# Optimization experiments

Measured on AMD Instinct MI355X. Metric: run time of the kernel, lower is better.

Reference implementation:

```python
import jax, jax.numpy as jnp
import numpy as np

N_NODES = 100000
N_EDGES = 1600000
N_GRAPHS = 256
NODE_DIM = 64
EDGE_DIM = 64
HIDDEN = 128
VOCAB = 128
N_CONV = 3
R_MIN, R_MAX = 1.0, 6.0
LN_EPS = 1e-5


def layer_norm(x, g, b):
    mu = jnp.mean(x, axis=-1, keepdims=True)
    var = jnp.mean(jnp.square(x - mu), axis=-1, keepdims=True)
    return (x - mu) * jax.lax.rsqrt(var + LN_EPS) * g + b


def setup_inputs() -> dict:
    key = jax.random.key(0)
    ks = jax.random.split(key, 16)
    inp = {}
    inp["numbers"] = jax.random.randint(ks[0], (N_NODES,), 0, VOCAB)
    inp["edge_index"] = jax.random.randint(ks[1], (2, N_EDGES), 0, N_NODES)
    inp["edge_length"] = jax.random.uniform(ks[2], (N_EDGES,), minval=R_MIN, maxval=R_MAX, dtype=jnp.float32)
    inp["batch"] = jnp.sort(jax.random.randint(ks[3], (N_NODES,), 0, N_GRAPHS))
    s = 0.1
    inp["embed_table"] = jax.random.normal(ks[4], (VOCAB, NODE_DIM), jnp.float32)
    inp["Wf"] = jax.random.normal(ks[5], (N_CONV, 2 * NODE_DIM + EDGE_DIM, NODE_DIM), jnp.float32) * s
    inp["bf"] = jnp.zeros((N_CONV, NODE_DIM), jnp.float32)
    inp["Ws"] = jax.random.normal(ks[6], (N_CONV, 2 * NODE_DIM + EDGE_DIM, NODE_DIM), jnp.float32) * s
    inp["bs"] = jnp.zeros((N_CONV, NODE_DIM), jnp.float32)
    inp["ln_g"] = jnp.ones((N_CONV, NODE_DIM), jnp.float32)
    inp["ln_b"] = jnp.zeros((N_CONV, NODE_DIM), jnp.float32)
    inp["olp_W1"] = jax.random.normal(ks[7], (NODE_DIM, HIDDEN), jnp.float32) * s
    inp["olp_b1"] = jnp.zeros((HIDDEN,), jnp.float32)
    inp["olp_g1"] = jnp.ones((HIDDEN,), jnp.float32)
    inp["olp_bt1"] = jnp.zeros((HIDDEN,), jnp.float32)
    inp["olp_W2"] = jax.random.normal(ks[8], (HIDDEN, HIDDEN), jnp.float32) * s
    inp["olp_b2"] = jnp.zeros((HIDDEN,), jnp.float32)
    inp["olp_g2"] = jnp.ones((HIDDEN,), jnp.float32)
    inp["olp_bt2"] = jnp.zeros((HIDDEN,), jnp.float32)
    inp["W_out"] = jax.random.normal(ks[9], (HIDDEN, 1), jnp.float32) * s
    inp["b_out"] = jnp.zeros((1,), jnp.float32)
    return inp


def reference(numbers, edge_index, edge_length, batch, embed_table,
              Wf, bf, Ws, bs, ln_g, ln_b,
              olp_W1, olp_b1, olp_g1, olp_bt1,
              olp_W2, olp_b2, olp_g2, olp_bt2,
              W_out, b_out):
    n_nodes = numbers.shape[0]
    # Gaussian edge expansion: exp(-0.5*((d - centers)/step)^2)  -> [E, edge_dim]
    centers = jnp.linspace(R_MIN, R_MAX, EDGE_DIM, dtype=jnp.float32)
    step = (R_MAX - R_MIN) / EDGE_DIM
    edge_attrs = jnp.exp(-0.5 * jnp.square((edge_length[:, None] - centers) / step))

    x = embed_table[numbers]                      # [N, node_dim]
    src, tgt = edge_index[0], edge_index[1]

    for i in range(N_CONV):
        z = jnp.concatenate([x[src], x[tgt], edge_attrs], axis=-1)  # [E, 2d+e]
        gate = jax.nn.sigmoid(z @ Wf[i] + bf[i]) * jax.nn.softplus(z @ Ws[i] + bs[i])
        msg = jax.ops.segment_sum(gate, src, num_segments=n_nodes)  # reduce='add'
        x = x + layer_norm(msg, ln_g[i], ln_b[i])

    # hidden OLPs: Linear -> LayerNorm -> Softplus (dropout identity at eval)
    h = jax.nn.softplus(layer_norm(x @ olp_W1 + olp_b1, olp_g1, olp_bt1))
    h = jax.nn.softplus(layer_norm(h @ olp_W2 + olp_b2, olp_g2, olp_bt2))
    e = h @ W_out + b_out                          # [N, 1]

    # per_atom_target=True -> segment mean over graphs
    sums = jax.ops.segment_sum(e, batch, num_segments=N_GRAPHS)      # [G, 1]
    cnt = jax.ops.segment_sum(jnp.ones((n_nodes,), e.dtype), batch, num_segments=N_GRAPHS)
    energy = sums / jnp.maximum(cnt, 1.0)[:, None]
    return energy
```

## Files before the change

kernel.cpp:

```cpp
#include <hip/hip_runtime.h>
#include <hip/hip_fp16.h>
#include <math.h>

#define NNODES 100000
#define NEDGES 1600000
#define NGRAPH 256
#define NCONV  3
#define TBL    4096
#define CHUNK  512
#define NCHUNK 196
#define R_MIN_ 1.0f
#define R_MAX_ 6.0f
#define LOG2E  1.4426950408889634f

typedef _Float16 h2t __attribute__((ext_vector_type(2)));
typedef _Float16 f16x8 __attribute__((ext_vector_type(8)));
typedef float f32x4 __attribute__((ext_vector_type(4)));
union H4 { float4 f4; __half2 q[4]; h2t h[4]; };
union HF { float4 f4; f16x8 h8; __half2 q[4]; };

__device__ __forceinline__ float softplus_f(float x){
  return fmaxf(x, 0.f) + __logf(1.f + __expf(-fabsf(x)));
}

__global__ void k_init(int* ccnt, float* gsum, int* gcnt){
  int i = blockIdx.x*256 + threadIdx.x;
  if (i < 256) ccnt[i] = 0;
  if (i < NGRAPH){ gsum[i] = 0.f; gcnt[i] = 0; }
}

__global__ void k_embed(const int* __restrict__ numbers, const float* __restrict__ embed,
                        float* __restrict__ x){
  int i = blockIdx.x*256 + threadIdx.x;
  if (i >= NNODES*64) return;
  int n = i >> 6, c = i & 63;
  x[i] = embed[numbers[n]*64 + c];
}

__global__ void k_lut(float2* __restrict__ lutg){
  __shared__ float sv[513], cv[513];
  int t = threadIdx.x;
  for (int i = t; i < 513; i += 256){
    float z = -16.f + (float)i * (1.f/16.f);
    sv[i] = 1.f / (1.f + exp2f(-z));
    float a = (float)i * (1.f/32.f);
    cv[i] = log2f(1.f + exp2f(-a));
  }
  __syncthreads();
  for (int i = t; i < 512; i += 256){
    lutg[i]       = make_float2(sv[i], sv[i+1]-sv[i]);
    lutg[512 + i] = make_float2(cv[i], cv[i+1]-cv[i]);
  }
}

__global__ void k_cnt(const int* __restrict__ src, int* ccnt){
  __shared__ int l[NCHUNK];
  int t = threadIdx.x;
  int e0 = blockIdx.x * 2048;
  if (t < NCHUNK) l[t] = 0;
  __syncthreads();
  #pragma unroll
  for (int k = 0; k < 8; k++){
    int e = e0 + k*256 + t;
    if (e < NEDGES) atomicAdd(&l[src[e] / CHUNK], 1);
  }
  __syncthreads();
  if (t < NCHUNK && l[t] > 0) atomicAdd(&ccnt[t], l[t]);
}

__global__ void k_cscan(const int* __restrict__ ccnt, int* __restrict__ cbase,
                        int* __restrict__ ccur, int* __restrict__ offs){
  __shared__ int s[256];
  int t = threadIdx.x;
  int v = (t < NCHUNK) ? ccnt[t] : 0;
  s[t] = v;
  __syncthreads();
  #pragma unroll
  for (int d = 1; d < 256; d <<= 1){
    int u = (t >= d) ? s[t-d] : 0;
    __syncthreads();
    s[t] += u;
    __syncthreads();
  }
  int excl = s[t] - v;
  if (t < NCHUNK){ cbase[t] = excl; ccur[t] = excl; }
  if (t == 0){ cbase[NCHUNK] = NEDGES; offs[NNODES] = NEDGES; }
}

__global__ void k_bin(const int* __restrict__ src, const int* __restrict__ tgt,
                      const float* __restrict__ elen, int* ccur,
                      int2* __restrict__ eb){
  __shared__ int lcnt[NCHUNK];
  __shared__ int lbase[NCHUNK];
  __shared__ int loff[NCHUNK];
  int t = threadIdx.x;
  int e0 = blockIdx.x * 2048;
  if (t < NCHUNK){ lcnt[t] = 0; loff[t] = 0; }
  __syncthreads();
  #pragma unroll
  for (int k = 0; k < 8; k++){
    int e = e0 + k*256 + t;
    if (e < NEDGES) atomicAdd(&lcnt[src[e] / CHUNK], 1);
  }
  __syncthreads();
  if (t < NCHUNK && lcnt[t] > 0) lbase[t] = atomicAdd(&ccur[t], lcnt[t]);
  __syncthreads();
  #pragma unroll
  for (int k = 0; k < 8; k++){
    int e = e0 + k*256 + t;
    if (e < NEDGES){
      int s = src[e];
      int c = s / CHUNK;
      int r = atomicAdd(&loff[c], 1);
      float key = (elen[e] - R_MIN_) * ((float)(TBL-1)/(R_MAX_-R_MIN_));
      key = fmaxf(key, 0.f);
      int idx = (int)(key + 0.5f);
      if (idx > TBL-1) idx = TBL-1;
      eb[lbase[c] + r] = make_int2(((s & (CHUNK-1)) << 17) | tgt[e], idx);
    }
  }
}

__global__ void k_fine(const int* __restrict__ cbase, const int2* __restrict__ eb,
                       int2* __restrict__ ep, int* __restrict__ offs){
  __shared__ int lcnt[CHUNK];
  __shared__ int lsc[CHUNK];
  int c = blockIdx.x;
  int t = threadIdx.x;
  int n0 = c * CHUNK;
  int n1 = min(n0 + CHUNK, NNODES);
  int cnt = n1 - n0;
  int j0 = cbase[c], j1 = cbase[c+1];
  lcnt[t] = 0;
  __syncthreads();
  for (int e = j0 + t; e < j1; e += 512)
    atomicAdd(&lcnt[((unsigned)eb[e].x) >> 17], 1);
  __syncthreads();
  lsc[t] = lcnt[t];
  __syncthreads();
  for (int d = 1; d < 512; d <<= 1){
    int v = (t >= d) ? lsc[t-d] : 0;
    __syncthreads();
    lsc[t] += v;
    __syncthreads();
  }
  int excl = lsc[t] - lcnt[t];
  if (t < cnt) offs[n0 + t] = j0 + excl;
  __syncthreads();
  lcnt[t] = j0 + excl;
  __syncthreads();
  for (int e = j0 + t; e < j1; e += 512){
    int2 rec = eb[e];
    int sl = ((unsigned)rec.x) >> 17;
    int pos = atomicAdd(&lcnt[sl], 1);
    ep[pos] = make_int2(rec.x & 0x1FFFF, rec.y);
  }
}

__global__ void k_gauss(const float* __restrict__ Wf, const float* __restrict__ bf,
                        const float* __restrict__ Ws, const float* __restrict__ bs,
                        __half* __restrict__ Gth){
  __shared__ float attr[64];
  int bi = blockIdx.x;
  int i = bi / TBL, r = bi % TBL;
  int t = threadIdx.x;
  float d = R_MIN_ + (R_MAX_-R_MIN_) * (float)r / (float)(TBL-1);
  if (t < 64){
    float cj = 1.f + 5.f * (float)t / 63.f;
    float u = (d - cj) * (64.f/5.f);
    attr[t] = __expf(-0.5f*u*u);
  }
  __syncthreads();
  int c = t >> 1;
  int side = t & 1;
  const float* W = (side ? Ws : Wf) + i*192*64 + 128*64 + c;
  float acc = (side ? bs : bf)[i*64 + c];
  #pragma unroll 8
  for (int j = 0; j < 64; j++) acc = fmaf(attr[j], W[j*64], acc);
  Gth[((size_t)i*TBL + r)*128 + t] = __float2half_rn(acc * LOG2E);
}

__global__ void k_wcat(const float* __restrict__ Wf, const float* __restrict__ Ws,
                       __half2* __restrict__ Wch){
  int idx = blockIdx.x*256 + threadIdx.x;
  if (idx >= 3*32*256) return;
  int i = idx / (32*256);
  int rem = idx % (32*256);
  int kp = rem >> 8, c = rem & 255;
  int p = (c < 128) ? (c >> 1) : ((c - 128) >> 1);
  int rbase = (c < 128) ? 0 : 64;
  const float* W = ((c & 1) ? Ws : Wf) + i*192*64;
  float v0 = W[(rbase + 2*kp  )*64 + p];
  float v1 = W[(rbase + 2*kp+1)*64 + p];
  Wch[idx] = __floats2half2_rn(v0, v1);
}

__global__ void k_wm(const float* __restrict__ W1, const float* __restrict__ W2,
                     __half* __restrict__ Wm1, __half* __restrict__ Wm2){
  int i = blockIdx.x*256 + threadIdx.x;
  if (i < 8192){
    int ct = i >> 10;
    int kt = (i >> 9) & 1;
    int lane = (i >> 3) & 63;
    int e = i & 7;
    int k = kt*32 + (lane>>4)*8 + e;
    int c = ct*16 + (lane&15);
    Wm1[i] = __float2half_rn(W1[k*128 + c]);
  }
  if (i < 16384){
    int ct = i >> 11;
    int kt = (i >> 9) & 3;
    int lane = (i >> 3) & 63;
    int e = i & 7;
    int k = kt*32 + (lane>>4)*8 + e;
    int c = ct*16 + (lane&15);
    Wm2[i] = __float2half_rn(W2[k*128 + c]);
  }
}

__global__ void k_ntrans(const float* __restrict__ x, const __half2* __restrict__ Wch,
                         __half2* __restrict__ pqh){
  __shared__ __half2 xh[32*32];
  int n0 = blockIdx.x * 32;
  int t = threadIdx.x;
  {
    const float4* xp = (const float4*)(x + (size_t)n0*64);
    float4 a = xp[2*t], b = xp[2*t+1];
    H4 hh;
    hh.q[0] = __float22half2_rn(make_float2(a.x, a.y));
    hh.q[1] = __float22half2_rn(make_float2(a.z, a.w));
    hh.q[2] = __float22half2_rn(make_float2(b.x, b.y));
    hh.q[3] = __float22half2_rn(make_float2(b.z, b.w));
    *(float4*)(xh + 4*t) = hh.f4;
  }
  __syncthreads();
  int cg = t & 63, ng = t >> 6;
  float4 acc[8];
  #pragma unroll
  for (int i = 0; i < 8; i++) acc[i] = make_float4(0.f,0.f,0.f,0.f);
  const __half2* wp = Wch + 4*cg;
  const __half2* xbase = xh + ng*8*32;
  for (int kp = 0; kp < 32; kp += 4){
    H4 w[4];
    #pragma unroll
    for (int j = 0; j < 4; j++) w[j].f4 = *(const float4*)(wp + (kp+j)*256);
    #pragma unroll
    for (int nn = 0; nn < 8; nn++){
      H4 xv; xv.f4 = *(const float4*)(xbase + nn*32 + kp);
      #pragma unroll
      for (int j = 0; j < 4; j++){
        acc[nn].x = __builtin_amdgcn_fdot2(xv.h[j], w[j].h[0], acc[nn].x, false);
        acc[nn].y = __builtin_amdgcn_fdot2(xv.h[j], w[j].h[1], acc[nn].y, false);
        acc[nn].z = __builtin_amdgcn_fdot2(xv.h[j], w[j].h[2], acc[nn].z, false);
        acc[nn].w = __builtin_amdgcn_fdot2(xv.h[j], w[j].h[3], acc[nn].w, false);
      }
    }
  }
  #pragma unroll
  for (int nn = 0; nn < 8; nn++){
    int node = n0 + ng*8 + nn;
    __half2 h0 = __float22half2_rn(make_float2(acc[nn].x*LOG2E, acc[nn].y*LOG2E));
    __half2 h1 = __float22half2_rn(make_float2(acc[nn].z*LOG2E, acc[nn].w*LOG2E));
    __half2* dst = pqh + (size_t)node*128 + 2*cg;
    dst[0] = h0; dst[1] = h1;
  }
}

__global__ void k_edge(const __half2* __restrict__ pqh,
                       const int* __restrict__ offs, const int2* __restrict__ ep,
                       const __half* __restrict__ Gth, const float* __restrict__ lng,
                       const float* __restrict__ lnb, const float2* __restrict__ lutg,
                       float* __restrict__ x){
  __shared__ float2 lut[1024];
  {
    float4* d = (float4*)lut;
    const float4* s = (const float4*)lutg;
    d[threadIdx.x]       = s[threadIdx.x];
    d[threadIdx.x + 256] = s[threadIdx.x + 256];
  }
  __syncthreads();
  int wid  = (blockIdx.x*256 + threadIdx.x) >> 6;
  int lane = threadIdx.x & 63;
  int n = wid;
  int j0 = __builtin_amdgcn_readfirstlane(offs[n]);
  int j1 = __builtin_amdgcn_readfirstlane(offs[n+1]);
  int nfull = (j1 - j0) >> 3;
  int2 eb8[8];
  if (nfull > 0){
    #pragma unroll
    for (int i = 0; i < 8; i++) eb8[i] = ep[j0 + i];
  }
  float2 pp = __half22float2(pqh[(size_t)n*128 + lane]);
  float pf = pp.x, ps = pp.y;
  const char* pqb = (const char*)pqh;
  const char* gtb = (const char*)Gth;
  unsigned qob = 256u + ((unsigned)lane << 2);
  unsigned lob = (unsigned)lane << 2;
  float acc = 0.f;
  int u = j0;
  for (int b = 0; b < nfull; b++){
    __half2 qr[8], gr[8];
    #pragma unroll
    for (int i = 0; i < 8; i++){
      qr[i] = *(const __half2*)(pqb + ((((unsigned)eb8[i].x) << 9) + qob));
      gr[i] = *(const __half2*)(gtb + ((((unsigned)eb8[i].y) << 8) + lob));
    }
    if (b + 1 < nfull){
      #pragma unroll
      for (int i = 0; i < 8; i++) eb8[i] = ep[u + 8 + i];
    }
    #pragma unroll
    for (int i = 0; i < 8; i++){
      float2 z = __half22float2(__hadd2(qr[i], gr[i]));
      float zf = pf + z.x;
      float xi = fmaf(fmaxf(fminf(zf, 15.96f), -16.f), 16.f, 256.f);
      int i1 = (int)xi;
      float f1 = __builtin_amdgcn_fractf(xi);
      float2 e1 = lut[i1];
      float sig = fmaf(e1.y, f1, e1.x);
      float zs = ps + z.y;
      float xj = fminf(fabsf(zs), 15.96f) * 32.f;
      int i2 = (int)xj;
      float f2 = __builtin_amdgcn_fractf(xj);
      float2 e2 = lut[512 + i2];
      float sp = fmaxf(zs, 0.f) + fmaf(e2.y, f2, e2.x);
      acc = fmaf(sig, sp, acc);
    }
    u += 8;
  }
  for (; u < j1; u++){
    int2 e = ep[u];
    __half2 q = *(const __half2*)(pqb + ((((unsigned)e.x) << 9) + qob));
    __half2 g = *(const __half2*)(gtb + ((((unsigned)e.y) << 8) + lob));
    float2 z = __half22float2(__hadd2(q, g));
    float zf = pf + z.x;
    float xi = fmaf(fmaxf(fminf(zf, 15.96f), -16.f), 16.f, 256.f);
    int i1 = (int)xi;
    float f1 = __builtin_amdgcn_fractf(xi);
    float2 e1 = lut[i1];
    float sig = fmaf(e1.y, f1, e1.x);
    float zs = ps + z.y;
    float xj = fminf(fabsf(zs), 15.96f) * 32.f;
    int i2 = (int)xj;
    float f2 = __builtin_amdgcn_fractf(xj);
    float2 e2 = lut[512 + i2];
    float sp = fmaxf(zs, 0.f) + fmaf(e2.y, f2, e2.x);
    acc = fmaf(sig, sp, acc);
  }
  float s1 = acc, s2 = acc*acc;
  #pragma unroll
  for (int o = 32; o > 0; o >>= 1){ s1 += __shfl_xor(s1, o, 64); s2 += __shfl_xor(s2, o, 64); }
  float mu  = s1 * (1.f/64.f);
  float var = s2 * (1.f/64.f) - mu*mu;
  float inv = rsqrtf(fmaxf(var, 0.f) + 1e-5f);
  float y = (acc - mu) * inv * lng[lane] + lnb[lane];
  x[(size_t)n*64 + lane] += y;
}

__global__ void k_head(const float* __restrict__ x,
                       const __half* __restrict__ Wm1, const float* __restrict__ b1,
                       const float* __restrict__ g1, const float* __restrict__ bt1,
                       const __half* __restrict__ Wm2, const float* __restrict__ b2,
                       const float* __restrict__ g2, const float* __restrict__ bt2,
                       const float* __restrict__ Wout, const int* __restrict__ batch,
                       float* gsum, int* gcnt){
  __shared__ __half xh[32*72];
  __shared__ __half hs[32*136];
  __shared__ float red[4][32][2];
  __shared__ float stat[32][2];
  __shared__ float es[32];
  int n0 = blockIdx.x * 32;
  int t = threadIdx.x;
  int w = t >> 6, lane = t & 63;
  int lg = lane >> 4, lc = lane & 15;
  int col0 = w*32 + lc, col1 = w*32 + 16 + lc;

  {
    int n = t >> 3, g = t & 7;
    const float4* xp = (const float4*)(x + (size_t)(n0 + n)*64 + g*8);
    float4 a = xp[0], b = xp[1];
    HF hh;
    hh.q[0] = __float22half2_rn(make_float2(a.x, a.y));
    hh.q[1] = __float22half2_rn(make_float2(a.z, a.w));
    hh.q[2] = __float22half2_rn(make_float2(b.x, b.y));
    hh.q[3] = __float22half2_rn(make_float2(b.z, b.w));
    *(float4*)(xh + n*72 + g*8) = hh.f4;
  }
  __syncthreads();

  f32x4 acc[2][2];
  {
    HF a[2][2], b[2][2];
    #pragma unroll
    for (int m = 0; m < 2; m++)
      #pragma unroll
      for (int kt = 0; kt < 2; kt++)
        a[m][kt].f4 = *(const float4*)(xh + (m*16 + lc)*72 + kt*32 + lg*8);
    const float4* wb = (const float4*)Wm1;
    #pragma unroll
    for (int ct = 0; ct < 2; ct++)
      #pragma unroll
      for (int kt = 0; kt < 2; kt++)
        b[ct][kt].f4 = wb[(((w*2 + ct)*2 + kt)*64) + lane];
    #pragma unroll
    for (int m = 0; m < 2; m++)
      #pragma unroll
      for (int ct = 0; ct < 2; ct++){
        f32x4 c = {0.f, 0.f, 0.f, 0.f};
        c = __builtin_amdgcn_mfma_f32_16x16x32_f16(a[m][0].h8, b[ct][0].h8, c, 0, 0, 0);
        c = __builtin_amdgcn_mfma_f32_16x16x32_f16(a[m][1].h8, b[ct][1].h8, c, 0, 0, 0);
        acc[m][ct] = c;
      }
  }
  {
    float bv0 = b1[col0], bv1 = b1[col1];
    #pragma unroll
    for (int m = 0; m < 2; m++)
      #pragma unroll
      for (int r = 0; r < 4; r++){
        acc[m][0][r] += bv0; acc[m][1][r] += bv1;
        float a0 = acc[m][0][r], a1 = acc[m][1][r];
        float s1 = a0 + a1, s2 = a0*a0 + a1*a1;
        #pragma unroll
        for (int o = 1; o < 16; o <<= 1){ s1 += __shfl_xor(s1, o, 64); s2 += __shfl_xor(s2, o, 64); }
        if (lc == 0){ int row = m*16 + lg*4 + r; red[w][row][0] = s1; red[w][row][1] = s2; }
      }
  }
  __syncthreads();
  if (t < 32){
    float s1 = red[0][t][0] + red[1][t][0] + red[2][t][0] + red[3][t][0];
    float s2 = red[0][t][1] + red[1][t][1] + red[2][t][1] + red[3][t][1];
    float mu = s1 * (1.f/128.f);
    float var = s2 * (1.f/128.f) - mu*mu;
    stat[t][0] = mu;
    stat[t][1] = rsqrtf(fmaxf(var, 0.f) + 1e-5f);
  }
  __syncthreads();
  {
    float g1a = g1[col0], g1b = g1[col1], b1a = bt1[col0], b1b = bt1[col1];
    #pragma unroll
    for (int m = 0; m < 2; m++)
      #pragma unroll
      for (int r = 0; r < 4; r++){
        int row = m*16 + lg*4 + r;
        float mu = stat[row][0], inv = stat[row][1];
        float y0 = (acc[m][0][r] - mu)*inv*g1a + b1a;
        float y1 = (acc[m][1][r] - mu)*inv*g1b + b1b;
        hs[row*136 + col0] = __float2half_rn(softplus_f(y0));
        hs[row*136 + col1] = __float2half_rn(softplus_f(y1));
      }
  }
  __syncthreads();

  f32x4 acc2[2][2];
  {
    HF b[2][4];
    const float4* wb = (const float4*)Wm2;
    #pragma unroll
    for (int ct = 0; ct < 2; ct++)
      #pragma unroll
      for (int kt = 0; kt < 4; kt++)
        b[ct][kt].f4 = wb[(((w*2 + ct)*4 + kt)*64) + lane];
    #pragma unroll
    for (int m = 0; m < 2; m++){
      f32x4 c0 = {0.f,0.f,0.f,0.f}, c1 = {0.f,0.f,0.f,0.f};
      #pragma unroll
      for (int kt = 0; kt < 4; kt++){
        HF av; av.f4 = *(const float4*)(hs + (m*16 + lc)*136 + kt*32 + lg*8);
        c0 = __builtin_amdgcn_mfma_f32_16x16x32_f16(av.h8, b[0][kt].h8, c0, 0, 0, 0);
        c1 = __builtin_amdgcn_mfma_f32_16x16x32_f16(av.h8, b[1][kt].h8, c1, 0, 0, 0);
      }
      acc2[m][0] = c0; acc2[m][1] = c1;
    }
  }
  {
    float bv0 = b2[col0], bv1 = b2[col1];
    #pragma unroll
    for (int m = 0; m < 2; m++)
      #pragma unroll
      for (int r = 0; r < 4; r++){
        acc2[m][0][r] += bv0; acc2[m][1][r] += bv1;
        float a0 = acc2[m][0][r], a1 = acc2[m][1][r];
        float s1 = a0 + a1, s2 = a0*a0 + a1*a1;
        #pragma unroll
        for (int o = 1; o < 16; o <<= 1){ s1 += __shfl_xor(s1, o, 64); s2 += __shfl_xor(s2, o, 64); }
        if (lc == 0){ int row = m*16 + lg*4 + r; red[w][row][0] = s1; red[w][row][1] = s2; }
      }
  }
  __syncthreads();
  if (t < 32){
    float s1 = red[0][t][0] + red[1][t][0] + red[2][t][0] + red[3][t][0];
    float s2 = red[0][t][1] + red[1][t][1] + red[2][t][1] + red[3][t][1];
    float mu = s1 * (1.f/128.f);
    float var = s2 * (1.f/128.f) - mu*mu;
    stat[t][0] = mu;
    stat[t][1] = rsqrtf(fmaxf(var, 0.f) + 1e-5f);
  }
  __syncthreads();
  {
    float g2a = g2[col0], g2b = g2[col1], b2a = bt2[col0], b2b = bt2[col1];
    float woa = Wout[col0], wob = Wout[col1];
    #pragma unroll
    for (int m = 0; m < 2; m++)
      #pragma unroll
      for (int r = 0; r < 4; r++){
        int row = m*16 + lg*4 + r;
        float mu = stat[row][0], inv = stat[row][1];
        float e = softplus_f((acc2[m][0][r] - mu)*inv*g2a + b2a) * woa
                + softplus_f((acc2[m][1][r] - mu)*inv*g2b + b2b) * wob;
        #pragma unroll
        for (int o = 1; o < 16; o <<= 1) e += __shfl_xor(e, o, 64);
        if (lc == 0) red[w][row][0] = e;
      }
  }
  __syncthreads();
  if (t < 32) es[t] = red[0][t][0] + red[1][t][0] + red[2][t][0] + red[3][t][0];
  __syncthreads();

  if (t < 32){
    int node = n0 + t;
    int g = batch[node];
    bool head = (t == 0) || (batch[node-1] != g);
    if (head){
      float s = 0.f; int c = 0;
      int j = t;
      while (j < 32 && batch[n0+j] == g){ s += es[j]; c++; j++; }
      atomicAdd(&gsum[g], s);
      atomicAdd(&gcnt[g], c);
    }
  }
}

__global__ void k_final(const float* __restrict__ gsum, const int* __restrict__ gcnt,
                        const float* __restrict__ bout, float* __restrict__ out){
  int g = threadIdx.x;
  if (g < NGRAPH)
    out[g] = gsum[g] / fmaxf((float)gcnt[g], 1.f) + bout[0];
}

extern "C" void kernel_launch(void* const* d_in, const int* in_sizes, int n_in,
                              void* d_out, int out_size, void* d_ws, size_t ws_size,
                              hipStream_t stream){
  const int*   numbers = (const int*)d_in[0];
  const int*   eidx    = (const int*)d_in[1];
  const float* elen    = (const float*)d_in[2];
  const int*   batch   = (const int*)d_in[3];
  const float* embed   = (const float*)d_in[4];
  const float* Wf      = (const float*)d_in[5];
  const float* bf      = (const float*)d_in[6];
  const float* Ws      = (const float*)d_in[7];
  const float* bs      = (const float*)d_in[8];
  const float* lng     = (const float*)d_in[9];
  const float* lnb     = (const float*)d_in[10];
  const float* W1      = (const float*)d_in[11];
  const float* b1      = (const float*)d_in[12];
  const float* g1      = (const float*)d_in[13];
  const float* bt1     = (const float*)d_in[14];
  const float* W2      = (const float*)d_in[15];
  const float* b2      = (const float*)d_in[16];
  const float* g2      = (const float*)d_in[17];
  const float* bt2     = (const float*)d_in[18];
  const float* Wout    = (const float*)d_in[19];
  const float* bout    = (const float*)d_in[20];
  const int* src = eidx;
  const int* tgt = eidx + NEDGES;

  float*   x    = (float*)d_ws;
  __half2* pqh  = (__half2*)(x + (size_t)NNODES*64);
  __half*  Gth  = (__half*)(pqh + (size_t)NNODES*128);
  __half2* Wch  = (__half2*)(Gth + (size_t)3*TBL*128);
  __half*  Wm1  = (__half*)(Wch + (size_t)3*32*256);
  __half*  Wm2  = Wm1 + 8192;
  float2*  lutg = (float2*)(Wm2 + 16384);
  int2*    ep   = (int2*)(lutg + 1024);
  int2*    ebuf = ep + NEDGES;
  int*     offs = (int*)(ebuf + NEDGES);
  int*     ccnt = offs + NNODES + 1;
  int*     cbase= ccnt + 256;
  int*     ccur = cbase + 256;
  float*   gsum = (float*)(ccur + 256);
  int*     gcnt = (int*)(gsum + NGRAPH);
  float*   out  = (float*)d_out;

  k_init  <<<(NNODES+255)/256, 256, 0, stream>>>(ccnt, gsum, gcnt);
  k_embed <<<(NNODES*64+255)/256, 256, 0, stream>>>(numbers, embed, x);

  k_cnt   <<<(NEDGES+2047)/2048, 256, 0, stream>>>(src, ccnt);
  k_cscan <<<1, 256, 0, stream>>>(ccnt, cbase, ccur, offs);
  k_bin   <<<(NEDGES+2047)/2048, 256, 0, stream>>>(src, tgt, elen, ccur, ebuf);
  k_fine  <<<NCHUNK, 512, 0, stream>>>(cbase, ebuf, ep, offs);

  k_gauss <<<3*TBL, 128, 0, stream>>>(Wf, bf, Ws, bs, Gth);
  k_wcat  <<<(3*32*256+255)/256, 256, 0, stream>>>(Wf, Ws, Wch);
  k_wm    <<<64, 256, 0, stream>>>(W1, W2, Wm1, Wm2);
  k_lut   <<<1, 256, 0, stream>>>(lutg);

  for (int i = 0; i < NCONV; i++){
    k_ntrans<<<NNODES/32, 256, 0, stream>>>(x, Wch + (size_t)i*32*256, pqh);
    k_edge  <<<NNODES/4, 256, 0, stream>>>(pqh, offs, ep,
                                           Gth + (size_t)i*TBL*128,
                                           lng + i*64, lnb + i*64, lutg, x);
  }

  k_head<<<NNODES/32, 256, 0, stream>>>(x, Wm1, b1, g1, bt1,
                                        Wm2, b2, g2, bt2, Wout, batch, gsum, gcnt);
  k_final<<<1, 256, 0, stream>>>(gsum, gcnt, bout, out);
}
```

Baseline: 639.0 us.

## Use MFMA for node transform and simplify edge LUT indexing

The per-node projection in k_ntrans moves from packed fdot2 loops to 16x16x32 f16 MFMA instructions, with weights repacked into the MFMA B-fragment layout and node features staged in padded shared memory. In the edge loop, the sigmoid and softplus LUT lookups fold the offset and scale into one fma plus a med3 clamp, and the softplus table is rebuilt so that softplus becomes max(z, table). This cuts per-edge ALU work in the hot loop. The new softplus formulation and the fp16 MFMA change rounding slightly compared with before.

```diff
diff --git a/kernel.cpp b/kernel.cpp
--- a/kernel.cpp
+++ b/kernel.cpp
@@ -13,10 +13,8 @@
 #define R_MAX_ 6.0f
 #define LOG2E  1.4426950408889634f
 
-typedef _Float16 h2t __attribute__((ext_vector_type(2)));
 typedef _Float16 f16x8 __attribute__((ext_vector_type(8)));
 typedef float f32x4 __attribute__((ext_vector_type(4)));
-union H4 { float4 f4; __half2 q[4]; h2t h[4]; };
 union HF { float4 f4; f16x8 h8; __half2 q[4]; };
 
 __device__ __forceinline__ float softplus_f(float x){
@@ -43,8 +41,7 @@
   for (int i = t; i < 513; i += 256){
     float z = -16.f + (float)i * (1.f/16.f);
     sv[i] = 1.f / (1.f + exp2f(-z));
-    float a = (float)i * (1.f/32.f);
-    cv[i] = log2f(1.f + exp2f(-a));
+    cv[i] = log2f(1.f + exp2f(z));
   }
   __syncthreads();
   for (int i = t; i < 512; i += 256){
@@ -181,18 +178,22 @@
 }
 
 __global__ void k_wcat(const float* __restrict__ Wf, const float* __restrict__ Ws,
-                       __half2* __restrict__ Wch){
+                       __half* __restrict__ WmC){
   int idx = blockIdx.x*256 + threadIdx.x;
-  if (idx >= 3*32*256) return;
-  int i = idx / (32*256);
-  int rem = idx % (32*256);
-  int kp = rem >> 8, c = rem & 255;
-  int p = (c < 128) ? (c >> 1) : ((c - 128) >> 1);
-  int rbase = (c < 128) ? 0 : 64;
-  const float* W = ((c & 1) ? Ws : Wf) + i*192*64;
-  float v0 = W[(rbase + 2*kp  )*64 + p];
-  float v1 = W[(rbase + 2*kp+1)*64 + p];
-  Wch[idx] = __floats2half2_rn(v0, v1);
+  if (idx >= 3*16384) return;
+  int i = idx / 16384;
+  int rem = idx & 16383;
+  int ct = rem >> 10;
+  int kt = (rem >> 9) & 1;
+  int lane = (rem >> 3) & 63;
+  int e = rem & 7;
+  int col = ct*16 + (lane & 15);
+  int part = col >> 6;
+  int ch = col & 63;
+  int k = kt*32 + (lane >> 4)*8 + e;
+  int row = ((part >> 1) ? 64 : 0) + k;
+  const float* W = ((part & 1) ? Ws : Wf) + i*192*64;
+  WmC[idx] = __float2half_rn(W[row*64 + ch]);
 }
 
 __global__ void k_wm(const float* __restrict__ W1, const float* __restrict__ W2,
@@ -218,52 +219,58 @@
   }
 }
 
-__global__ void k_ntrans(const float* __restrict__ x, const __half2* __restrict__ Wch,
+__global__ void k_ntrans(const float* __restrict__ x, const __half* __restrict__ WmC,
                          __half2* __restrict__ pqh){
-  __shared__ __half2 xh[32*32];
+  __shared__ __half xh[32*72];
   int n0 = blockIdx.x * 32;
   int t = threadIdx.x;
-  {
-    const float4* xp = (const float4*)(x + (size_t)n0*64);
-    float4 a = xp[2*t], b = xp[2*t+1];
-    H4 hh;
+  int w = t >> 6, lane = t & 63;
+  int lg = lane >> 4, lc = lane & 15;
+  {
+    int n = t >> 3, g = t & 7;
+    const float4* xp = (const float4*)(x + (size_t)(n0 + n)*64 + g*8);
+    float4 a = xp[0], b = xp[1];
+    HF hh;
     hh.q[0] = __float22half2_rn(make_float2(a.x, a.y));
     hh.q[1] = __float22half2_rn(make_float2(a.z, a.w));
     hh.q[2] = __float22half2_rn(make_float2(b.x, b.y));
     hh.q[3] = __float22half2_rn(make_float2(b.z, b.w));
-    *(float4*)(xh + 4*t) = hh.f4;
-  }
-  __syncthreads();
-  int cg = t & 63, ng = t >> 6;
-  float4 acc[8];
-  #pragma unroll
-  for (int i = 0; i < 8; i++) acc[i] = make_float4(0.f,0.f,0.f,0.f);
-  const __half2* wp = Wch + 4*cg;
-  const __half2* xbase = xh + ng*8*32;
-  for (int kp = 0; kp < 32; kp += 4){
-    H4 w[4];
-    #pragma unroll
-    for (int j = 0; j < 4; j++) w[j].f4 = *(const float4*)(wp + (kp+j)*256);
-    #pragma unroll
-    for (int nn = 0; nn < 8; nn++){
-      H4 xv; xv.f4 = *(const float4*)(xbase + nn*32 + kp);
-      #pragma unroll
-      for (int j = 0; j < 4; j++){
-        acc[nn].x = __builtin_amdgcn_fdot2(xv.h[j], w[j].h[0], acc[nn].x, false);
-        acc[nn].y = __builtin_amdgcn_fdot2(xv.h[j], w[j].h[1], acc[nn].y, false);
-        acc[nn].z = __builtin_amdgcn_fdot2(xv.h[j], w[j].h[2], acc[nn].z, false);
-        acc[nn].w = __builtin_amdgcn_fdot2(xv.h[j], w[j].h[3], acc[nn].w, false);
-      }
-    }
-  }
-  #pragma unroll
-  for (int nn = 0; nn < 8; nn++){
-    int node = n0 + ng*8 + nn;
-    __half2 h0 = __float22half2_rn(make_float2(acc[nn].x*LOG2E, acc[nn].y*LOG2E));
-    __half2 h1 = __float22half2_rn(make_float2(acc[nn].z*LOG2E, acc[nn].w*LOG2E));
-    __half2* dst = pqh + (size_t)node*128 + 2*cg;
-    dst[0] = h0; dst[1] = h1;
-  }
+    *(float4*)(xh + n*72 + g*8) = hh.f4;
+  }
+  __syncthreads();
+  HF a[2][2];
+  #pragma unroll
+  for (int m = 0; m < 2; m++)
+    #pragma unroll
+    for (int kt = 0; kt < 2; kt++)
+      a[m][kt].f4 = *(const float4*)(xh + (m*16 + lc)*72 + kt*32 + lg*8);
+  const float4* wb = (const float4*)WmC;
+  f32x4 acc[4][2];
+  #pragma unroll
+  for (int p4 = 0; p4 < 4; p4++){
+    int ct = p4*4 + w;
+    HF b0, b1;
+    b0.f4 = wb[(ct*2 + 0)*64 + lane];
+    b1.f4 = wb[(ct*2 + 1)*64 + lane];
+    #pragma unroll
+    for (int m = 0; m < 2; m++){
+      f32x4 c = {0.f, 0.f, 0.f, 0.f};
+      c = __builtin_amdgcn_mfma_f32_16x16x32_f16(a[m][0].h8, b0.h8, c, 0, 0, 0);
+      c = __builtin_amdgcn_mfma_f32_16x16x32_f16(a[m][1].h8, b1.h8, c, 0, 0, 0);
+      acc[p4][m] = c;
+    }
+  }
+  #pragma unroll
+  for (int m = 0; m < 2; m++)
+    #pragma unroll
+    for (int r = 0; r < 4; r++){
+      int node = n0 + m*16 + lg*4 + r;
+      int ch = w*16 + lc;
+      __half2 hp = __floats2half2_rn(acc[0][m][r]*LOG2E, acc[1][m][r]*LOG2E);
+      __half2 hq = __floats2half2_rn(acc[2][m][r]*LOG2E, acc[3][m][r]*LOG2E);
+      pqh[(size_t)node*128 + ch]      = hp;
+      pqh[(size_t)node*128 + 64 + ch] = hq;
+    }
 }
 
 __global__ void k_edge(const __half2* __restrict__ pqh,
@@ -291,7 +298,9 @@
     for (int i = 0; i < 8; i++) eb8[i] = ep[j0 + i];
   }
   float2 pp = __half22float2(pqh[(size_t)n*128 + lane]);
-  float pf = pp.x, ps = pp.y;
+  float pfo = fmaf(pp.x, 16.f, 256.f);
+  float pso = fmaf(pp.y, 16.f, 768.f);
+  float ps = pp.y;
   const char* pqb = (const char*)pqh;
   const char* gtb = (const char*)Gth;
   unsigned qob = 256u + ((unsigned)lane << 2);
@@ -312,18 +321,17 @@
     #pragma unroll
     for (int i = 0; i < 8; i++){
       float2 z = __half22float2(__hadd2(qr[i], gr[i]));
-      float zf = pf + z.x;
-      float xi = fmaf(fmaxf(fminf(zf, 15.96f), -16.f), 16.f, 256.f);
+      float xi = __builtin_amdgcn_fmed3f(fmaf(z.x, 16.f, pfo), 0.f, 511.36f);
       int i1 = (int)xi;
       float f1 = __builtin_amdgcn_fractf(xi);
       float2 e1 = lut[i1];
       float sig = fmaf(e1.y, f1, e1.x);
-      float zs = ps + z.y;
-      float xj = fminf(fabsf(zs), 15.96f) * 32.f;
+      float xj = __builtin_amdgcn_fmed3f(fmaf(z.y, 16.f, pso), 512.f, 1023.36f);
       int i2 = (int)xj;
       float f2 = __builtin_amdgcn_fractf(xj);
-      float2 e2 = lut[512 + i2];
-      float sp = fmaxf(zs, 0.f) + fmaf(e2.y, f2, e2.x);
+      float2 e2 = lut[i2];
+      float zs = ps + z.y;
+      float sp = fmaxf(zs, fmaf(e2.y, f2, e2.x));
       acc = fmaf(sig, sp, acc);
     }
     u += 8;
@@ -333,18 +341,17 @@
     __half2 q = *(const __half2*)(pqb + ((((unsigned)e.x) << 9) + qob));
     __half2 g = *(const __half2*)(gtb + ((((unsigned)e.y) << 8) + lob));
     float2 z = __half22float2(__hadd2(q, g));
-    float zf = pf + z.x;
-    float xi = fmaf(fmaxf(fminf(zf, 15.96f), -16.f), 16.f, 256.f);
+    float xi = __builtin_amdgcn_fmed3f(fmaf(z.x, 16.f, pfo), 0.f, 511.36f);
     int i1 = (int)xi;
     float f1 = __builtin_amdgcn_fractf(xi);
     float2 e1 = lut[i1];
     float sig = fmaf(e1.y, f1, e1.x);
-    float zs = ps + z.y;
-    float xj = fminf(fabsf(zs), 15.96f) * 32.f;
+    float xj = __builtin_amdgcn_fmed3f(fmaf(z.y, 16.f, pso), 512.f, 1023.36f);
     int i2 = (int)xj;
     float f2 = __builtin_amdgcn_fractf(xj);
-    float2 e2 = lut[512 + i2];
-    float sp = fmaxf(zs, 0.f) + fmaf(e2.y, f2, e2.x);
+    float2 e2 = lut[i2];
+    float zs = ps + z.y;
+    float sp = fmaxf(zs, fmaf(e2.y, f2, e2.x));
     acc = fmaf(sig, sp, acc);
   }
   float s1 = acc, s2 = acc*acc;
@@ -568,8 +575,8 @@
   float*   x    = (float*)d_ws;
   __half2* pqh  = (__half2*)(x + (size_t)NNODES*64);
   __half*  Gth  = (__half*)(pqh + (size_t)NNODES*128);
-  __half2* Wch  = (__half2*)(Gth + (size_t)3*TBL*128);
-  __half*  Wm1  = (__half*)(Wch + (size_t)3*32*256);
+  __half*  WmC  = Gth + (size_t)3*TBL*128;
+  __half*  Wm1  = WmC + (size_t)3*16384;
   __half*  Wm2  = Wm1 + 8192;
   float2*  lutg = (float2*)(Wm2 + 16384);
   int2*    ep   = (int2*)(lutg + 1024);
@@ -591,12 +598,12 @@
   k_fine  <<<NCHUNK, 512, 0, stream>>>(cbase, ebuf, ep, offs);
 
   k_gauss <<<3*TBL, 128, 0, stream>>>(Wf, bf, Ws, bs, Gth);
-  k_wcat  <<<(3*32*256+255)/256, 256, 0, stream>>>(Wf, Ws, Wch);
+  k_wcat  <<<(3*16384+255)/256, 256, 0, stream>>>(Wf, Ws, WmC);
   k_wm    <<<64, 256, 0, stream>>>(W1, W2, Wm1, Wm2);
   k_lut   <<<1, 256, 0, stream>>>(lutg);
 
   for (int i = 0; i < NCONV; i++){
-    k_ntrans<<<NNODES/32, 256, 0, stream>>>(x, Wch + (size_t)i*32*256, pqh);
+    k_ntrans<<<NNODES/32, 256, 0, stream>>>(x, WmC + (size_t)i*16384, pqh);
     k_edge  <<<NNODES/4, 256, 0, stream>>>(pqh, offs, ep,
                                            Gth + (size_t)i*TBL*128,
                                            lng + i*64, lnb + i*64, lutg, x);
```

After: 577.0 us. 9.7% less time.
